# Performance work log

Hardware: AMD Instinct MI355X
Metric: run time of the kernel (lower is better)

Reference implementation:

```python
import jax, jax.numpy as jnp
import numpy as np

D_MODEL = 1024
N_HEADS = 16
D_HEAD = 64
B, S = 2, 2048


def setup_inputs() -> dict:
    key = jax.random.key(0)
    ks = jax.random.split(key, 16)
    HDH = N_HEADS * D_HEAD
    s = 0.02
    return {
        "h": jax.random.normal(ks[0], (B, S, D_MODEL), dtype=jnp.float32),
        "att_mask": jax.random.randint(ks[1], (B, S), 0, 2) > 0,
        "Wq": jax.random.normal(ks[2], (D_MODEL, HDH), dtype=jnp.float32) * s,
        "bq": jnp.zeros((HDH,), dtype=jnp.float32),
        "Wkv": jax.random.normal(ks[3], (D_MODEL, 2 * HDH), dtype=jnp.float32) * s,
        "bkv": jnp.zeros((2 * HDH,), dtype=jnp.float32),
        "Wo": jax.random.normal(ks[4], (HDH, D_MODEL), dtype=jnp.float32) * s,
        "bo": jnp.zeros((D_MODEL,), dtype=jnp.float32),
        "W1": jax.random.normal(ks[5], (D_MODEL, D_MODEL), dtype=jnp.float32) * s,
        "b1": jnp.zeros((D_MODEL,), dtype=jnp.float32),
        "W2": jax.random.normal(ks[6], (D_MODEL, D_MODEL), dtype=jnp.float32) * s,
        "b2": jnp.zeros((D_MODEL,), dtype=jnp.float32),
        "ln_g": jnp.ones((D_MODEL,), dtype=jnp.float32),
        "ln_b": jnp.zeros((D_MODEL,), dtype=jnp.float32),
    }


def _layer_norm(x, g, b, eps=1e-6):
    mu = jnp.mean(x, axis=-1, keepdims=True)
    var = jnp.mean(jnp.square(x - mu), axis=-1, keepdims=True)
    return (x - mu) * jax.lax.rsqrt(var + eps) * g + b


def reference(h, att_mask, Wq, bq, Wkv, bkv, Wo, bo, W1, b1, W2, b2, ln_g, ln_b):
    bz, ln, _ = h.shape
    scale = 1.0 / (D_HEAD ** 0.5)
    q = (h @ Wq + bq).reshape(bz, ln, N_HEADS, D_HEAD)
    kv = h @ Wkv + bkv
    k, v = jnp.split(kv, 2, axis=-1)
    k = k.reshape(bz, ln, N_HEADS, D_HEAD)
    v = v.reshape(bz, ln, N_HEADS, D_HEAD)
    # scores: [b, heads, len_q, len_k]
    scores = jnp.einsum('bqhd,bkhd->bhqk', q, k) * scale
    scores = jnp.where(att_mask[:, None, None, :], -1e9, scores)
    probs = jax.nn.softmax(scores, axis=-1)
    att = jnp.einsum('bhqk,bkhd->bqhd', probs, v).reshape(bz, ln, N_HEADS * D_HEAD)
    att_out = att @ Wo + bo
    # glu_type == 1
    g = jax.nn.sigmoid(h @ W1 + b1) * (h @ W2 + b2)
    return _layer_norm(h + att_out + g, ln_g, ln_b)
```

## Files before the change

kernel.cpp:

```cpp
#include <hip/hip_runtime.h>
#include <hip/hip_bf16.h>


typedef short bf16x8 __attribute__((ext_vector_type(8)));
typedef float f32x4  __attribute__((ext_vector_type(4)));
typedef float f32x16 __attribute__((ext_vector_type(16)));
typedef unsigned int u32x4 __attribute__((ext_vector_type(4)));

typedef const __attribute__((address_space(1))) void* gas_cvp;
typedef __attribute__((address_space(3))) void* las_vp;

__device__ __forceinline__ void gload_lds16(const void* g, void* l) {
  __builtin_amdgcn_global_load_lds((gas_cvp)g, (las_vp)l, 16, 0, 0);
}

__device__ __forceinline__ short f2bf(float f) {
  __hip_bfloat16 h = __float2bfloat16(f);
  return *reinterpret_cast<short*>(&h);
}
__device__ __forceinline__ float bf2f(short s) {
  unsigned u = ((unsigned)(unsigned short)s) << 16;
  return __builtin_bit_cast(float, u);
}

#if __has_builtin(__builtin_amdgcn_exp2f)
#define EXP2(x) __builtin_amdgcn_exp2f(x)
#else
#define EXP2(x) exp2f(x)
#endif

constexpr int BATCH = 2;
constexpr int SEQ   = 2048;
constexpr int NH    = 16;
constexpr int MROWS = BATCH * SEQ;
constexpr int NSPLIT = 4;
constexpr int KSPL   = SEQ / NSPLIT;
constexpr int RH     = MROWS * NH;


__global__ __launch_bounds__(256) void cvt_bf16(const float* __restrict__ src,
                                                short* __restrict__ dst, int n4) {
  int i = blockIdx.x * 256 + threadIdx.x;
  if (i >= n4) return;
  float4 v = reinterpret_cast<const float4*>(src)[i];
  short4 o;
  o.x = f2bf(v.x); o.y = f2bf(v.y); o.z = f2bf(v.z); o.w = f2bf(v.w);
  reinterpret_cast<short4*>(dst)[i] = o;
}

struct WtA {
  const float* s[6];
  short* d[6];
  int st[6];
};
__global__ __launch_bounds__(256) void wtrans6(WtA a) {
  __shared__ float tile[32][33];
  const float* __restrict__ src = a.s[blockIdx.z];
  short* __restrict__ dst = a.d[blockIdx.z];
  const int stride = a.st[blockIdx.z];
  const int tx = threadIdx.x & 31, ty = threadIdx.x >> 5;
  const int n0 = blockIdx.x * 32, k0 = blockIdx.y * 32;
  #pragma unroll
  for (int i = 0; i < 32; i += 8)
    tile[ty + i][tx] = src[(size_t)(k0 + ty + i) * stride + n0 + tx];
  __syncthreads();
  #pragma unroll
  for (int i = 0; i < 32; i += 8)
    dst[(size_t)(n0 + ty + i) * 1024 + k0 + tx] = f2bf(tile[tx][ty + i]);
}

__global__ __launch_bounds__(256) void vtrans(const short* __restrict__ qkv,
                                              short* __restrict__ vt) {
  __shared__ short tile[32][33];
  const int tx = threadIdx.x & 31, ty = threadIdx.x >> 5;
  const int s0 = blockIdx.x * 32, d0 = blockIdx.y * 32, b = blockIdx.z;
  #pragma unroll
  for (int i = 0; i < 32; i += 8)
    tile[ty + i][tx] = qkv[(size_t)(b * SEQ + s0 + ty + i) * 3072 + 2048 + d0 + tx];
  __syncthreads();
  #pragma unroll
  for (int i = 0; i < 32; i += 8)
    vt[(size_t)(b * 1024 + d0 + ty + i) * SEQ + s0 + tx] = tile[tx][ty + i];
}

__global__ void pack_bias(const float* __restrict__ bq, const float* __restrict__ bkv,
                          const float* __restrict__ b1, const float* __restrict__ b2,
                          float* __restrict__ bqkv, float* __restrict__ b12) {
  int i = blockIdx.x * 256 + threadIdx.x;
  if (i < 1024) bqkv[i] = bq[i];
  else if (i < 3072) bqkv[i] = bkv[i - 1024];
  else if (i < 4096) b12[i - 3072] = b1[i - 3072];
  else if (i < 5120) b12[i - 3072] = b2[i - 4096];
}

__device__ __forceinline__ bool mask_at(const void* mp, int idx, int flag) {
  if (flag == 1) return ((const int*)mp)[idx] != 0;
  if (flag == 2) return ((const float*)mp)[idx] != 0.f;
  return ((const unsigned char*)mp)[idx] != 0;
}

__global__ __launch_bounds__(256) void premask(const void* __restrict__ msk,
                                               float* __restrict__ mbL) {
  __shared__ int si, sf;
  const unsigned* m = (const unsigned*)msk;
  if (threadIdx.x == 0) { si = 1; sf = 1; }
  __syncthreads();
  bool oki = true, okf = true;
  for (int i = threadIdx.x; i < 1024; i += 256) {
    unsigned v = m[i];
    oki = oki && (v <= 1u);
    okf = okf && (v == 0u || v == 0x3F800000u);
  }
  if (!oki) si = 0;
  if (!okf) sf = 0;
  __syncthreads();
  const int flag = si ? 1 : (sf ? 2 : 0);
  int i = blockIdx.x * 256 + threadIdx.x;
  if (i < MROWS) mbL[i] = mask_at(msk, i, flag) ? -1.442695e9f : -8.0f;
}

__global__ __launch_bounds__(256) void gemm_kernel(const short* __restrict__ A,
                                                   const short* __restrict__ BT,
                                                   const float* __restrict__ bias,
                                                   short* __restrict__ outp, int N) {
  __shared__ short Alds[4096];
  __shared__ short Blds[4096];
  const int tid = threadIdx.x;
  const int w = tid >> 6, lane = tid & 63, g = lane >> 4, lr = lane & 15;
  const int wr = w >> 1, wc = w & 1;
  const int bm = blockIdx.y, bn = blockIdx.x;

  f32x4 acc[4][4] = {};

  const int srow = tid >> 2;
  const int scol = (tid & 3) * 8;
  const short* Ab = A  + (size_t)(bm * 128 + srow) * 1024 + scol;
  const short* Bb = BT + (size_t)(bn * 128 + srow) * 1024 + scol;

  for (int kt = 0; kt < 32; ++kt) {
    const int kb = kt * 32;
    __syncthreads();
    gload_lds16(Ab + kb,             &Alds[tid * 8]);
    gload_lds16(Ab + 64 * 1024 + kb, &Alds[2048 + tid * 8]);
    gload_lds16(Bb + kb,             &Blds[tid * 8]);
    gload_lds16(Bb + 64 * 1024 + kb, &Blds[2048 + tid * 8]);
    asm volatile("s_waitcnt vmcnt(0)" ::: "memory");
    __syncthreads();

    bf16x8 af[4], bfr[4];
    #pragma unroll
    for (int m = 0; m < 4; ++m)
      af[m] = *reinterpret_cast<const bf16x8*>(&Alds[(wr * 64 + m * 16 + lr) * 32 + g * 8]);
    #pragma unroll
    for (int n = 0; n < 4; ++n)
      bfr[n] = *reinterpret_cast<const bf16x8*>(&Blds[(wc * 64 + n * 16 + lr) * 32 + g * 8]);
    #pragma unroll
    for (int m = 0; m < 4; ++m)
      #pragma unroll
      for (int n = 0; n < 4; ++n)
        acc[m][n] = __builtin_amdgcn_mfma_f32_16x16x32_bf16(af[m], bfr[n], acc[m][n], 0, 0, 0);
  }

  #pragma unroll
  for (int m = 0; m < 4; ++m) {
    const int row = bm * 128 + wr * 64 + m * 16 + g * 4;
    #pragma unroll
    for (int n = 0; n < 4; ++n) {
      const int col = bn * 128 + wc * 64 + n * 16 + lr;
      const float bv = bias[col];
      #pragma unroll
      for (int r = 0; r < 4; ++r)
        outp[(size_t)(row + r) * N + col] = f2bf(acc[m][n][r] + bv);
    }
  }
}

__global__ __launch_bounds__(256) void glu_kernel(const short* __restrict__ x12,
                                                  short* __restrict__ g) {
  const int i = blockIdx.x * 256 + threadIdx.x;
  const int row = i >> 7, c8 = (i & 127) * 8;
  const size_t base = (size_t)row * 2048 + c8;
  bf16x8 a = *reinterpret_cast<const bf16x8*>(&x12[base]);
  bf16x8 b = *reinterpret_cast<const bf16x8*>(&x12[base + 1024]);
  bf16x8 r;
  #pragma unroll
  for (int j = 0; j < 8; ++j) {
    const float x = bf2f(a[j]);
    r[j] = f2bf(bf2f(b[j]) / (1.f + __expf(-x)));
  }
  *reinterpret_cast<bf16x8*>(&g[(size_t)row * 1024 + c8]) = r;
}

constexpr int KB = 128;
constexpr int KSLOT = 8 * 130;
constexpr int VSLOT = 16 * 65;

__global__ __launch_bounds__(256) void attn_kernel(const short* __restrict__ qkv,
                                                   const short* __restrict__ vt,
                                                   const float* __restrict__ mbL,
                                                   short* __restrict__ opart,
                                                   float* __restrict__ spart) {
  __shared__ short Kl[2][KSLOT * 8];
  __shared__ short Vl[2][VSLOT * 8];
  __shared__ float mb[KSPL];

  const int tid = threadIdx.x;
  const int w = tid >> 6, lane = tid & 63, ql = lane & 31, hi = lane >> 5;
  const int sp = blockIdx.x & (NSPLIT - 1), qb = blockIdx.x / NSPLIT;
  const int h = blockIdx.y, b = blockIdx.z;
  const int qrow = qb * 128 + w * 32 + ql;
  const int kofs = sp * KSPL;

  bf16x8 qf[4];
  {
    const short* qp = qkv + (size_t)(b * SEQ + qrow) * 3072 + h * 64;
    #pragma unroll
    for (int c = 0; c < 4; ++c)
      qf[c] = *reinterpret_cast<const bf16x8*>(qp + c * 16 + hi * 8);
  }

  const short* gkbase = qkv + (size_t)(b * SEQ + kofs) * 3072 + 1024 + h * 64
                        + (size_t)(tid >> 3) * 3072 + (tid & 7) * 8;
  const short* gvbase = vt + ((size_t)(b * 1024 + h * 64) + (tid >> 4)) * SEQ + kofs
                        + (tid & 15) * 8;
  short* kwr0 = &Kl[0][((tid & 7) * 130 + (tid >> 3)) * 8];
  short* vwr0 = &Vl[0][((tid & 15) * 65 + (tid >> 4)) * 8];

  u32x4 kreg0, kreg1, kreg2, kreg3, vreg0, vreg1, vreg2, vreg3;
  auto loadTile = [&](int kt) {
    const short* gk = gkbase + (size_t)kt * KB * 3072;
    kreg0 = *reinterpret_cast<const u32x4*>(gk);
    kreg1 = *reinterpret_cast<const u32x4*>(gk + 32 * 3072);
    kreg2 = *reinterpret_cast<const u32x4*>(gk + 64 * 3072);
    kreg3 = *reinterpret_cast<const u32x4*>(gk + 96 * 3072);
    const short* gv = gvbase + kt * KB;
    vreg0 = *reinterpret_cast<const u32x4*>(gv);
    vreg1 = *reinterpret_cast<const u32x4*>(gv + 16 * SEQ);
    vreg2 = *reinterpret_cast<const u32x4*>(gv + 32 * SEQ);
    vreg3 = *reinterpret_cast<const u32x4*>(gv + 48 * SEQ);
  };
  auto writeTile = [&](int buf) {
    short* kd = kwr0 + buf * KSLOT * 8;
    *reinterpret_cast<u32x4*>(kd)            = kreg0;
    *reinterpret_cast<u32x4*>(kd + 32 * 8)   = kreg1;
    *reinterpret_cast<u32x4*>(kd + 64 * 8)   = kreg2;
    *reinterpret_cast<u32x4*>(kd + 96 * 8)   = kreg3;
    short* vd = vwr0 + buf * VSLOT * 8;
    *reinterpret_cast<u32x4*>(vd)            = vreg0;
    *reinterpret_cast<u32x4*>(vd + 16 * 8)   = vreg1;
    *reinterpret_cast<u32x4*>(vd + 32 * 8)   = vreg2;
    *reinterpret_cast<u32x4*>(vd + 48 * 8)   = vreg3;
  };

  float s_run = 0.f;
  f32x16 oacc0 = {}, oacc1 = {};

  if (tid < 128) gload_lds16(mbL + b * SEQ + kofs + tid * 4, &mb[tid * 4]);
  loadTile(0);
  writeTile(0);
  __syncthreads();

  const short* krd0 = &Kl[0][(hi * 130 + ql) * 8];
  const short* vrd0 = &Vl[0][(hi * 65 + ql) * 8];

  constexpr int NT = KSPL / KB;
  for (int kt = 0; kt < NT; ++kt) {
    const int cur = kt & 1;
    if (kt + 1 < NT) loadTile(kt + 1);
    const short* Kb = krd0 + cur * KSLOT * 8;
    const short* Vb = vrd0 + cur * VSLOT * 8;

    #pragma unroll
    for (int t2 = 0; t2 < 4; ++t2) {
      f32x16 sc = {};
      __builtin_amdgcn_s_setprio(1);
      #pragma unroll
      for (int c = 0; c < 4; ++c) {
        bf16x8 kf = *reinterpret_cast<const bf16x8*>(Kb + (c * 260 + t2 * 32) * 8);
        sc = __builtin_amdgcn_mfma_f32_32x32x16_bf16(kf, qf[c], sc, 0, 0, 0);
      }
      __builtin_amdgcn_s_setprio(0);
      float p[16];
      #pragma unroll
      for (int u = 0; u < 4; ++u) {
        float4 m4 = *reinterpret_cast<const float4*>(&mb[kt * KB + t2 * 32 + u * 8 + hi * 4]);
        p[4 * u + 0] = EXP2(fmaf(sc[4 * u + 0], 0.18033688f, m4.x));
        p[4 * u + 1] = EXP2(fmaf(sc[4 * u + 1], 0.18033688f, m4.y));
        p[4 * u + 2] = EXP2(fmaf(sc[4 * u + 2], 0.18033688f, m4.z));
        p[4 * u + 3] = EXP2(fmaf(sc[4 * u + 3], 0.18033688f, m4.w));
      }
      {
        float a0 = (p[0] + p[1]) + (p[2] + p[3]);
        float a1 = (p[4] + p[5]) + (p[6] + p[7]);
        float a2 = (p[8] + p[9]) + (p[10] + p[11]);
        float a3 = (p[12] + p[13]) + (p[14] + p[15]);
        s_run += (a0 + a1) + (a2 + a3);
      }
      unsigned P[8];
      #pragma unroll
      for (int j = 0; j < 8; ++j)
        asm("v_cvt_pk_bf16_f32 %0, %1, %2" : "=v"(P[j]) : "v"(p[2 * j]), "v"(p[2 * j + 1]));
      asm("v_permlane32_swap_b32 %0, %1" : "+v"(P[0]), "+v"(P[2]));
      asm("v_permlane32_swap_b32 %0, %1" : "+v"(P[1]), "+v"(P[3]));
      asm("v_permlane32_swap_b32 %0, %1" : "+v"(P[4]), "+v"(P[6]));
      asm("v_permlane32_swap_b32 %0, %1" : "+v"(P[5]), "+v"(P[7]));
      u32x4 c0 = { P[0], P[1], P[2], P[3] };
      u32x4 c1 = { P[4], P[5], P[6], P[7] };
      bf16x8 pf[2] = { __builtin_bit_cast(bf16x8, c0), __builtin_bit_cast(bf16x8, c1) };

      __builtin_amdgcn_s_setprio(1);
      #pragma unroll
      for (int ch = 0; ch < 2; ++ch) {
        const int gb = (t2 * 4 + ch * 2) * 65;
        bf16x8 v0 = *reinterpret_cast<const bf16x8*>(Vb + gb * 8);
        bf16x8 v1 = *reinterpret_cast<const bf16x8*>(Vb + (gb + 32) * 8);
        oacc0 = __builtin_amdgcn_mfma_f32_32x32x16_bf16(v0, pf[ch], oacc0, 0, 0, 0);
        oacc1 = __builtin_amdgcn_mfma_f32_32x32x16_bf16(v1, pf[ch], oacc1, 0, 0, 0);
      }
      __builtin_amdgcn_s_setprio(0);
    }
    if (kt + 1 < NT) {
      writeTile(cur ^ 1);
      __syncthreads();
    }
  }

  const float sT = s_run + __shfl_xor(s_run, 32);
  const size_t obase = (size_t)sp * RH * 64 + (size_t)(b * SEQ + qrow) * 1024 + h * 64;
  #pragma unroll
  for (int dt = 0; dt < 2; ++dt) {
    #pragma unroll
    for (int u = 0; u < 4; ++u) {
      short4 st;
      const f32x16& oa = dt ? oacc1 : oacc0;
      st.x = f2bf(oa[4 * u + 0]);
      st.y = f2bf(oa[4 * u + 1]);
      st.z = f2bf(oa[4 * u + 2]);
      st.w = f2bf(oa[4 * u + 3]);
      *reinterpret_cast<short4*>(&opart[obase + dt * 32 + u * 8 + hi * 4]) = st;
    }
  }
  if (hi == 0)
    spart[sp * RH + (b * SEQ + qrow) * NH + h] = sT;
}

__global__ __launch_bounds__(256) void attn_merge(const short* __restrict__ opart,
                                                  const float* __restrict__ spart,
                                                  short* __restrict__ att) {
  const int idx = blockIdx.x * 256 + threadIdx.x;
  const int rh = idx >> 3;
  const size_t base = (size_t)rh * 64 + (idx & 7) * 8;
  float acc[8] = {};
  float ss = 0.f;
  #pragma unroll
  for (int s = 0; s < NSPLIT; ++s) {
    bf16x8 o = *reinterpret_cast<const bf16x8*>(&opart[(size_t)s * RH * 64 + base]);
    #pragma unroll
    for (int j = 0; j < 8; ++j) acc[j] += bf2f(o[j]);
    ss += spart[s * RH + rh];
  }
  const float inv = 1.f / ss;
  bf16x8 r;
  #pragma unroll
  for (int j = 0; j < 8; ++j) r[j] = f2bf(acc[j] * inv);
  *reinterpret_cast<bf16x8*>(&att[base]) = r;
}

__global__ __launch_bounds__(256) void ln_kernel(const float* __restrict__ h,
                                                 const short* __restrict__ ao,
                                                 const short* __restrict__ gl,
                                                 const float* __restrict__ gamma,
                                                 const float* __restrict__ beta,
                                                 float* __restrict__ out) {
  const int row = blockIdx.x;
  const size_t base = (size_t)row * 1024;
  const int t = threadIdx.x;
  __shared__ float red[4];
  float x[4];
  #pragma unroll
  for (int j = 0; j < 4; ++j) {
    const int c = t + j * 256;
    x[j] = h[base + c] + bf2f(ao[base + c]) + bf2f(gl[base + c]);
  }
  float s = x[0] + x[1] + x[2] + x[3];
  #pragma unroll
  for (int d = 1; d < 64; d <<= 1) s += __shfl_xor(s, d);
  if ((t & 63) == 0) red[t >> 6] = s;
  __syncthreads();
  const float mu = (red[0] + red[1] + red[2] + red[3]) * (1.f / 1024.f);
  __syncthreads();
  float vs = 0.f;
  #pragma unroll
  for (int j = 0; j < 4; ++j) { const float dx = x[j] - mu; vs += dx * dx; }
  #pragma unroll
  for (int d = 1; d < 64; d <<= 1) vs += __shfl_xor(vs, d);
  if ((t & 63) == 0) red[t >> 6] = vs;
  __syncthreads();
  const float var = (red[0] + red[1] + red[2] + red[3]) * (1.f / 1024.f);
  const float rs = rsqrtf(var + 1e-6f);
  #pragma unroll
  for (int j = 0; j < 4; ++j) {
    const int c = t + j * 256;
    out[base + c] = (x[j] - mu) * rs * gamma[c] + beta[c];
  }
}


extern "C" void kernel_launch(void* const* d_in, const int* in_sizes, int n_in,
                              void* d_out, int out_size, void* d_ws, size_t ws_size,
                              hipStream_t stream) {
  const float* h   = (const float*)d_in[0];
  const void*  msk = d_in[1];
  const float* Wq  = (const float*)d_in[2];
  const float* bq  = (const float*)d_in[3];
  const float* Wkv = (const float*)d_in[4];
  const float* bkv = (const float*)d_in[5];
  const float* Wo  = (const float*)d_in[6];
  const float* bo  = (const float*)d_in[7];
  const float* W1  = (const float*)d_in[8];
  const float* b1  = (const float*)d_in[9];
  const float* W2  = (const float*)d_in[10];
  const float* b2  = (const float*)d_in[11];
  const float* lng = (const float*)d_in[12];
  const float* lnb = (const float*)d_in[13];
  float* out = (float*)d_out;

  char* ws = (char*)d_ws;
  size_t off = 0;
  auto alloc = [&](size_t bytes) {
    char* p = ws + off;
    off += (bytes + 255) & ~(size_t)255;
    return p;
  };
  short* X     = (short*)alloc((size_t)MROWS * 1024 * 2);
  short* WqkvT = (short*)alloc((size_t)3072 * 1024 * 2);
  short* WoT   = (short*)alloc((size_t)1024 * 1024 * 2);
  short* W1T   = (short*)alloc((size_t)1024 * 1024 * 2);
  short* W2T   = (short*)alloc((size_t)1024 * 1024 * 2);
  float* bqkv  = (float*)alloc(3072 * 4);
  float* b12   = (float*)alloc(2048 * 4);
  float* MBL   = (float*)alloc((size_t)MROWS * 4);
  short* QKV   = (short*)alloc((size_t)MROWS * 3072 * 2);
  short* VT    = (short*)alloc((size_t)BATCH * 1024 * SEQ * 2);
  short* ATT   = (short*)alloc((size_t)MROWS * 1024 * 2);
  short* X1    = (short*)alloc((size_t)MROWS * 1024 * 2);
  short* AO    = (short*)alloc((size_t)MROWS * 1024 * 2);
  short* OP    = (short*)alloc((size_t)NSPLIT * RH * 64 * 2);
  float* SP    = (float*)alloc((size_t)NSPLIT * RH * 4);
  short* X12   = OP;
  if (off > ws_size) return;

  cvt_bf16<<<4096, 256, 0, stream>>>(h, X, MROWS * 1024 / 4);
  WtA wa;
  wa.s[0] = Wq;          wa.d[0] = WqkvT;                wa.st[0] = 1024;
  wa.s[1] = Wkv;         wa.d[1] = WqkvT + 1024 * 1024;  wa.st[1] = 2048;
  wa.s[2] = Wkv + 1024;  wa.d[2] = WqkvT + 2048 * 1024;  wa.st[2] = 2048;
  wa.s[3] = Wo;          wa.d[3] = WoT;                  wa.st[3] = 1024;
  wa.s[4] = W1;          wa.d[4] = W1T;                  wa.st[4] = 1024;
  wa.s[5] = W2;          wa.d[5] = W2T;                  wa.st[5] = 1024;
  wtrans6<<<dim3(32, 32, 6), 256, 0, stream>>>(wa);
  pack_bias<<<20, 256, 0, stream>>>(bq, bkv, b1, b2, bqkv, b12);
  premask<<<16, 256, 0, stream>>>(msk, MBL);

  gemm_kernel<<<dim3(24, 32), 256, 0, stream>>>(X, WqkvT, bqkv, QKV, 3072);
  vtrans<<<dim3(64, 32, 2), 256, 0, stream>>>(QKV, VT);
  attn_kernel<<<dim3(16 * NSPLIT, 16, 2), 256, 0, stream>>>(QKV, VT, MBL, OP, SP);
  attn_merge<<<RH * 8 / 256, 256, 0, stream>>>(OP, SP, ATT);
  gemm_kernel<<<dim3(16, 32), 256, 0, stream>>>(X, W1T, b12, X12, 2048);
  glu_kernel<<<MROWS * 1024 / 8 / 256, 256, 0, stream>>>(X12, X1);
  gemm_kernel<<<dim3(8, 32), 256, 0, stream>>>(ATT, WoT, bo, AO, 1024);
  ln_kernel<<<MROWS, 256, 0, stream>>>(h, AO, X1, lng, lnb, out);
}
```

Baseline: 186.7 us.

## Fuse GLU into interleaved W1/W2 GEMM epilogue and shrink attention key tile

Interleaves W1 and W2 columns (and their biases) in the transposed weight buffer so that each adjacent lane pair in the GEMM epilogue holds matching W1/W2 outputs. The GEMM then computes sigmoid(a)*b in the epilogue using a lane shuffle, which removes the separate GLU kernel and the round trip of the 2048-wide intermediate through memory. The attention kernel's K/V tile also shrinks from 128 to 64 keys, with LDS padding adjusted to match, which lowers LDS and register use per tile but doubles the number of tile iterations and barriers.

```diff
diff --git a/kernel.cpp b/kernel.cpp
--- a/kernel.cpp
+++ b/kernel.cpp
@@ -52,12 +52,15 @@
   const float* s[6];
   short* d[6];
   int st[6];
+  int mul[6];
+  int add[6];
 };
 __global__ __launch_bounds__(256) void wtrans6(WtA a) {
   __shared__ float tile[32][33];
   const float* __restrict__ src = a.s[blockIdx.z];
   short* __restrict__ dst = a.d[blockIdx.z];
   const int stride = a.st[blockIdx.z];
+  const int mul = a.mul[blockIdx.z], add = a.add[blockIdx.z];
   const int tx = threadIdx.x & 31, ty = threadIdx.x >> 5;
   const int n0 = blockIdx.x * 32, k0 = blockIdx.y * 32;
   #pragma unroll
@@ -66,7 +69,7 @@
   __syncthreads();
   #pragma unroll
   for (int i = 0; i < 32; i += 8)
-    dst[(size_t)(n0 + ty + i) * 1024 + k0 + tx] = f2bf(tile[tx][ty + i]);
+    dst[(size_t)((n0 + ty + i) * mul + add) * 1024 + k0 + tx] = f2bf(tile[tx][ty + i]);
 }
 
 __global__ __launch_bounds__(256) void vtrans(const short* __restrict__ qkv,
@@ -85,12 +88,15 @@
 
 __global__ void pack_bias(const float* __restrict__ bq, const float* __restrict__ bkv,
                           const float* __restrict__ b1, const float* __restrict__ b2,
-                          float* __restrict__ bqkv, float* __restrict__ b12) {
+                          float* __restrict__ bqkv, float* __restrict__ b12i) {
   int i = blockIdx.x * 256 + threadIdx.x;
   if (i < 1024) bqkv[i] = bq[i];
   else if (i < 3072) bqkv[i] = bkv[i - 1024];
-  else if (i < 4096) b12[i - 3072] = b1[i - 3072];
-  else if (i < 5120) b12[i - 3072] = b2[i - 4096];
+  else if (i < 4096) {
+    const int j = i - 3072;
+    b12i[2 * j] = b1[j];
+    b12i[2 * j + 1] = b2[j];
+  }
 }
 
 __device__ __forceinline__ bool mask_at(const void* mp, int idx, int flag) {
@@ -119,6 +125,7 @@
   if (i < MROWS) mbL[i] = mask_at(msk, i, flag) ? -1.442695e9f : -8.0f;
 }
 
+template <int EPI>
 __global__ __launch_bounds__(256) void gemm_kernel(const short* __restrict__ A,
                                                    const short* __restrict__ BT,
                                                    const float* __restrict__ bias,
@@ -169,31 +176,24 @@
       const int col = bn * 128 + wc * 64 + n * 16 + lr;
       const float bv = bias[col];
       #pragma unroll
-      for (int r = 0; r < 4; ++r)
-        outp[(size_t)(row + r) * N + col] = f2bf(acc[m][n][r] + bv);
+      for (int r = 0; r < 4; ++r) {
+        const float v = acc[m][n][r] + bv;
+        if constexpr (EPI == 0) {
+          outp[(size_t)(row + r) * N + col] = f2bf(v);
+        } else {
+          const float vp = __shfl_xor(v, 1);
+          if (!(lr & 1))
+            outp[(size_t)(row + r) * (N / 2) + (col >> 1)] =
+                f2bf(vp / (1.f + __expf(-v)));
+        }
+      }
     }
   }
 }
 
-__global__ __launch_bounds__(256) void glu_kernel(const short* __restrict__ x12,
-                                                  short* __restrict__ g) {
-  const int i = blockIdx.x * 256 + threadIdx.x;
-  const int row = i >> 7, c8 = (i & 127) * 8;
-  const size_t base = (size_t)row * 2048 + c8;
-  bf16x8 a = *reinterpret_cast<const bf16x8*>(&x12[base]);
-  bf16x8 b = *reinterpret_cast<const bf16x8*>(&x12[base + 1024]);
-  bf16x8 r;
-  #pragma unroll
-  for (int j = 0; j < 8; ++j) {
-    const float x = bf2f(a[j]);
-    r[j] = f2bf(bf2f(b[j]) / (1.f + __expf(-x)));
-  }
-  *reinterpret_cast<bf16x8*>(&g[(size_t)row * 1024 + c8]) = r;
-}
-
-constexpr int KB = 128;
-constexpr int KSLOT = 8 * 130;
-constexpr int VSLOT = 16 * 65;
+constexpr int KB = 64;
+constexpr int KSLOT = 8 * 66;
+constexpr int VSLOT = 8 * 66;
 
 __global__ __launch_bounds__(256) void attn_kernel(const short* __restrict__ qkv,
                                                    const short* __restrict__ vt,
@@ -221,35 +221,27 @@
 
   const short* gkbase = qkv + (size_t)(b * SEQ + kofs) * 3072 + 1024 + h * 64
                         + (size_t)(tid >> 3) * 3072 + (tid & 7) * 8;
-  const short* gvbase = vt + ((size_t)(b * 1024 + h * 64) + (tid >> 4)) * SEQ + kofs
-                        + (tid & 15) * 8;
-  short* kwr0 = &Kl[0][((tid & 7) * 130 + (tid >> 3)) * 8];
-  short* vwr0 = &Vl[0][((tid & 15) * 65 + (tid >> 4)) * 8];
-
-  u32x4 kreg0, kreg1, kreg2, kreg3, vreg0, vreg1, vreg2, vreg3;
+  const short* gvbase = vt + ((size_t)(b * 1024 + h * 64) + (tid >> 3)) * SEQ + kofs
+                        + (tid & 7) * 8;
+  short* kwr = &Kl[0][((tid & 7) * 66 + (tid >> 3)) * 8];
+  short* vwr = &Vl[0][((tid & 7) * 66 + (tid >> 3)) * 8];
+
+  u32x4 kreg0, kreg1, vreg0, vreg1;
   auto loadTile = [&](int kt) {
     const short* gk = gkbase + (size_t)kt * KB * 3072;
     kreg0 = *reinterpret_cast<const u32x4*>(gk);
     kreg1 = *reinterpret_cast<const u32x4*>(gk + 32 * 3072);
-    kreg2 = *reinterpret_cast<const u32x4*>(gk + 64 * 3072);
-    kreg3 = *reinterpret_cast<const u32x4*>(gk + 96 * 3072);
     const short* gv = gvbase + kt * KB;
     vreg0 = *reinterpret_cast<const u32x4*>(gv);
-    vreg1 = *reinterpret_cast<const u32x4*>(gv + 16 * SEQ);
-    vreg2 = *reinterpret_cast<const u32x4*>(gv + 32 * SEQ);
-    vreg3 = *reinterpret_cast<const u32x4*>(gv + 48 * SEQ);
+    vreg1 = *reinterpret_cast<const u32x4*>(gv + 32 * SEQ);
   };
   auto writeTile = [&](int buf) {
-    short* kd = kwr0 + buf * KSLOT * 8;
-    *reinterpret_cast<u32x4*>(kd)            = kreg0;
-    *reinterpret_cast<u32x4*>(kd + 32 * 8)   = kreg1;
-    *reinterpret_cast<u32x4*>(kd + 64 * 8)   = kreg2;
-    *reinterpret_cast<u32x4*>(kd + 96 * 8)   = kreg3;
-    short* vd = vwr0 + buf * VSLOT * 8;
-    *reinterpret_cast<u32x4*>(vd)            = vreg0;
-    *reinterpret_cast<u32x4*>(vd + 16 * 8)   = vreg1;
-    *reinterpret_cast<u32x4*>(vd + 32 * 8)   = vreg2;
-    *reinterpret_cast<u32x4*>(vd + 48 * 8)   = vreg3;
+    short* kd = kwr + buf * KSLOT * 8;
+    *reinterpret_cast<u32x4*>(kd)          = kreg0;
+    *reinterpret_cast<u32x4*>(kd + 32 * 8) = kreg1;
+    short* vd = vwr + buf * VSLOT * 8;
+    *reinterpret_cast<u32x4*>(vd)          = vreg0;
+    *reinterpret_cast<u32x4*>(vd + 32 * 8) = vreg1;
   };
 
   float s_run = 0.f;
@@ -260,23 +252,23 @@
   writeTile(0);
   __syncthreads();
 
-  const short* krd0 = &Kl[0][(hi * 130 + ql) * 8];
-  const short* vrd0 = &Vl[0][(hi * 65 + ql) * 8];
+  const short* krd = &Kl[0][(hi * 66 + ql) * 8];
+  const short* vrd = &Vl[0][(hi * 66 + ql) * 8];
 
   constexpr int NT = KSPL / KB;
   for (int kt = 0; kt < NT; ++kt) {
     const int cur = kt & 1;
     if (kt + 1 < NT) loadTile(kt + 1);
-    const short* Kb = krd0 + cur * KSLOT * 8;
-    const short* Vb = vrd0 + cur * VSLOT * 8;
-
-    #pragma unroll
-    for (int t2 = 0; t2 < 4; ++t2) {
+    const short* Kb = krd + cur * KSLOT * 8;
+    const short* Vb = vrd + cur * VSLOT * 8;
+
+    #pragma unroll
+    for (int t2 = 0; t2 < 2; ++t2) {
       f32x16 sc = {};
       __builtin_amdgcn_s_setprio(1);
       #pragma unroll
       for (int c = 0; c < 4; ++c) {
-        bf16x8 kf = *reinterpret_cast<const bf16x8*>(Kb + (c * 260 + t2 * 32) * 8);
+        bf16x8 kf = *reinterpret_cast<const bf16x8*>(Kb + (c * 132 + t2 * 32) * 8);
         sc = __builtin_amdgcn_mfma_f32_32x32x16_bf16(kf, qf[c], sc, 0, 0, 0);
       }
       __builtin_amdgcn_s_setprio(0);
@@ -311,7 +303,7 @@
       __builtin_amdgcn_s_setprio(1);
       #pragma unroll
       for (int ch = 0; ch < 2; ++ch) {
-        const int gb = (t2 * 4 + ch * 2) * 65;
+        const int gb = (t2 * 4 + ch * 2) * 66;
         bf16x8 v0 = *reinterpret_cast<const bf16x8*>(Vb + gb * 8);
         bf16x8 v1 = *reinterpret_cast<const bf16x8*>(Vb + (gb + 32) * 8);
         oacc0 = __builtin_amdgcn_mfma_f32_32x32x16_bf16(v0, pf[ch], oacc0, 0, 0, 0);
@@ -319,6 +311,7 @@
       }
       __builtin_amdgcn_s_setprio(0);
     }
+
     if (kt + 1 < NT) {
       writeTile(cur ^ 1);
       __syncthreads();
@@ -435,10 +428,9 @@
   short* X     = (short*)alloc((size_t)MROWS * 1024 * 2);
   short* WqkvT = (short*)alloc((size_t)3072 * 1024 * 2);
   short* WoT   = (short*)alloc((size_t)1024 * 1024 * 2);
-  short* W1T   = (short*)alloc((size_t)1024 * 1024 * 2);
-  short* W2T   = (short*)alloc((size_t)1024 * 1024 * 2);
+  short* W12T  = (short*)alloc((size_t)2048 * 1024 * 2);
   float* bqkv  = (float*)alloc(3072 * 4);
-  float* b12   = (float*)alloc(2048 * 4);
+  float* b12i  = (float*)alloc(2048 * 4);
   float* MBL   = (float*)alloc((size_t)MROWS * 4);
   short* QKV   = (short*)alloc((size_t)MROWS * 3072 * 2);
   short* VT    = (short*)alloc((size_t)BATCH * 1024 * SEQ * 2);
@@ -447,27 +439,25 @@
   short* AO    = (short*)alloc((size_t)MROWS * 1024 * 2);
   short* OP    = (short*)alloc((size_t)NSPLIT * RH * 64 * 2);
   float* SP    = (float*)alloc((size_t)NSPLIT * RH * 4);
-  short* X12   = OP;
   if (off > ws_size) return;
 
   cvt_bf16<<<4096, 256, 0, stream>>>(h, X, MROWS * 1024 / 4);
   WtA wa;
-  wa.s[0] = Wq;          wa.d[0] = WqkvT;                wa.st[0] = 1024;
-  wa.s[1] = Wkv;         wa.d[1] = WqkvT + 1024 * 1024;  wa.st[1] = 2048;
-  wa.s[2] = Wkv + 1024;  wa.d[2] = WqkvT + 2048 * 1024;  wa.st[2] = 2048;
-  wa.s[3] = Wo;          wa.d[3] = WoT;                  wa.st[3] = 1024;
-  wa.s[4] = W1;          wa.d[4] = W1T;                  wa.st[4] = 1024;
-  wa.s[5] = W2;          wa.d[5] = W2T;                  wa.st[5] = 1024;
+  wa.s[0] = Wq;          wa.d[0] = WqkvT;                wa.st[0] = 1024;  wa.mul[0] = 1; wa.add[0] = 0;
+  wa.s[1] = Wkv;         wa.d[1] = WqkvT + 1024 * 1024;  wa.st[1] = 2048;  wa.mul[1] = 1; wa.add[1] = 0;
+  wa.s[2] = Wkv + 1024;  wa.d[2] = WqkvT + 2048 * 1024;  wa.st[2] = 2048;  wa.mul[2] = 1; wa.add[2] = 0;
+  wa.s[3] = Wo;          wa.d[3] = WoT;                  wa.st[3] = 1024;  wa.mul[3] = 1; wa.add[3] = 0;
+  wa.s[4] = W1;          wa.d[4] = W12T;                 wa.st[4] = 1024;  wa.mul[4] = 2; wa.add[4] = 0;
+  wa.s[5] = W2;          wa.d[5] = W12T;                 wa.st[5] = 1024;  wa.mul[5] = 2; wa.add[5] = 1;
   wtrans6<<<dim3(32, 32, 6), 256, 0, stream>>>(wa);
-  pack_bias<<<20, 256, 0, stream>>>(bq, bkv, b1, b2, bqkv, b12);
+  pack_bias<<<16, 256, 0, stream>>>(bq, bkv, b1, b2, bqkv, b12i);
   premask<<<16, 256, 0, stream>>>(msk, MBL);
 
-  gemm_kernel<<<dim3(24, 32), 256, 0, stream>>>(X, WqkvT, bqkv, QKV, 3072);
+  gemm_kernel<0><<<dim3(24, 32), 256, 0, stream>>>(X, WqkvT, bqkv, QKV, 3072);
   vtrans<<<dim3(64, 32, 2), 256, 0, stream>>>(QKV, VT);
   attn_kernel<<<dim3(16 * NSPLIT, 16, 2), 256, 0, stream>>>(QKV, VT, MBL, OP, SP);
   attn_merge<<<RH * 8 / 256, 256, 0, stream>>>(OP, SP, ATT);
-  gemm_kernel<<<dim3(16, 32), 256, 0, stream>>>(X, W1T, b12, X12, 2048);
-  glu_kernel<<<MROWS * 1024 / 8 / 256, 256, 0, stream>>>(X12, X1);
-  gemm_kernel<<<dim3(8, 32), 256, 0, stream>>>(ATT, WoT, bo, AO, 1024);
+  gemm_kernel<1><<<dim3(16, 32), 256, 0, stream>>>(X, W12T, b12i, X1, 2048);
+  gemm_kernel<0><<<dim3(8, 32), 256, 0, stream>>>(ATT, WoT, bo, AO, 1024);
   ln_kernel<<<MROWS, 256, 0, stream>>>(h, AO, X1, lng, lnb, out);
 }
```

After: 179.0 us. 1.04x faster.
